# Performance work log

Measured on AMD Instinct MI355X. Metric: run time of the kernel, lower is better.

Reference implementation:

```python
import jax, jax.numpy as jnp
import numpy as np

S, N, D, H = 4096, 16384, 768, 768  # n_slots, n_inputs, feature_size(=dim), mlp hidden
ITERS = 3
SCALE = D ** -0.5
LN_EPS = 1e-5  # torch LayerNorm default


def _ln(x, g, b):
    m = jnp.mean(x, axis=-1, keepdims=True)
    v = jnp.var(x, axis=-1, keepdims=True)
    return (x - m) * jax.lax.rsqrt(v + LN_EPS) * g + b


def setup_inputs() -> dict:
    key = jax.random.key(0)
    ks = jax.random.split(key, 16)
    w = lambda k, shp: jax.random.normal(k, shp, dtype=jnp.float32) * 0.02
    return {
        "cand_feat": jax.random.normal(ks[0], (S, D), dtype=jnp.float32),
        "pano_feat": jax.random.normal(ks[1], (N, D), dtype=jnp.float32),
        "Wq": w(ks[2], (D, D)), "bq": jnp.zeros((D,), jnp.float32),
        "Wk": w(ks[3], (D, D)), "bk": jnp.zeros((D,), jnp.float32),
        "Wv": w(ks[4], (D, D)), "bv": jnp.zeros((D,), jnp.float32),
        "W_ih": w(ks[5], (3 * D, D)), "b_ih": jnp.zeros((3 * D,), jnp.float32),
        "W_hh": w(ks[6], (3 * D, D)), "b_hh": jnp.zeros((3 * D,), jnp.float32),
        "W1": w(ks[7], (H, D)), "b1": jnp.zeros((H,), jnp.float32),
        "W2": w(ks[8], (D, H)), "b2": jnp.zeros((D,), jnp.float32),
        "g_in": jnp.ones((D,), jnp.float32), "be_in": jnp.zeros((D,), jnp.float32),
        "g_sl": jnp.ones((D,), jnp.float32), "be_sl": jnp.zeros((D,), jnp.float32),
        "g_ff": jnp.ones((D,), jnp.float32), "be_ff": jnp.zeros((D,), jnp.float32),
    }


def reference(cand_feat, pano_feat, Wq, bq, Wk, bk, Wv, bv,
              W_ih, b_ih, W_hh, b_hh, W1, b1, W2, b2,
              g_in, be_in, g_sl, be_sl, g_ff, be_ff):
    # dropout layers act as identity at inference
    slots = cand_feat                       # [S, D]
    pano = _ln(pano_feat, g_in, be_in)      # [N, D]
    k = pano @ Wk.T + bk                    # [N, D]
    v = pano @ Wv.T + bv                    # [N, D]
    for _ in range(ITERS):
        slots_prev = slots
        q = _ln(slots, g_sl, be_sl) @ Wq.T + bq          # [S, D]
        dots = jnp.einsum('id,jd->ij', q, k) * SCALE     # [S, N]
        attn = jax.nn.softmax(dots, axis=1)
        updates = jnp.einsum('jd,ij->id', v, attn)       # [S, D]
        # torch.nn.GRUCell(updates, slots_prev)
        gx = updates @ W_ih.T + b_ih                     # [S, 3D]
        gh = slots_prev @ W_hh.T + b_hh                  # [S, 3D]
        xr, xz, xn = jnp.split(gx, 3, axis=-1)
        hr, hz, hn = jnp.split(gh, 3, axis=-1)
        r = jax.nn.sigmoid(xr + hr)
        z = jax.nn.sigmoid(xz + hz)
        n = jnp.tanh(xn + r * hn)
        h = (1.0 - z) * n + z * slots_prev               # [S, D]
        ff = _ln(h, g_ff, be_ff)
        slots = h + (jax.nn.relu(ff @ W1.T + b1) @ W2.T + b2)
    return slots
```

## Files before the change

kernel.cpp:

```cpp
#include <hip/hip_runtime.h>
#include <cstdint>
#include <cstddef>

typedef __bf16 bf16;
typedef __bf16 bf16x8 __attribute__((ext_vector_type(8)));
typedef __bf16 bf16x4 __attribute__((ext_vector_type(4)));
typedef float f32x4 __attribute__((ext_vector_type(4)));
typedef long long i64;

#define S_DIM 4096
#define N_DIM 16384
#define D_DIM 768
#define NCHUNK 8192
#define NZ 8
#define KSLICE (NCHUNK / NZ)

static constexpr float SCALE = 0.03608439182435161f;

__device__ inline void gl_lds16(const void* g, void* l) {
  __builtin_amdgcn_global_load_lds((const __attribute__((address_space(1))) void*)g,
                                   (__attribute__((address_space(3))) void*)l, 16, 0, 0);
}

__device__ inline unsigned char to_fp8(float x) {
  int p = __builtin_amdgcn_cvt_pk_fp8_f32(x, x, 0, false);
  return (unsigned char)(p & 0xff);
}

struct GemmArgs {
  const bf16* A; const bf16* B;
  const float* bias;
  float* outF; bf16* outB; unsigned char* outP8;
  const float* res;
  float* lsum;
  int M, N, K, lda, ldb;
  float scale;
};

template<int EPIL>
__device__ __forceinline__ void gemm_core(const GemmArgs& g, const int bm, const int bn,
                                          bf16* sA, bf16* sB) {
  const int tid  = threadIdx.x;
  const int wave = tid >> 6;
  const int lane = tid & 63;
  const int quad = lane >> 4;
  const int l15  = lane & 15;
  const int wm = (wave >> 1) * 64;
  const int wn = (wave & 1) * 64;

  f32x4 acc[4][4];
#pragma unroll
  for (int t = 0; t < 4; ++t)
#pragma unroll
    for (int u = 0; u < 4; ++u) acc[t][u] = (f32x4){0.f, 0.f, 0.f, 0.f};

  const int s0 = wave * 64 + lane;
  const int s1 = 256 + s0;
  const size_t lda = (size_t)g.lda, ldb = (size_t)g.ldb;
  const bf16* gA0 = g.A + (size_t)(bm + (s0 >> 2)) * lda + (s0 & 3) * 8;
  const bf16* gA1 = g.A + (size_t)(bm + (s1 >> 2)) * lda + (s1 & 3) * 8;
  const bf16* gB0 = g.B + (size_t)(bn + (s0 >> 2)) * ldb + (s0 & 3) * 8;
  const bf16* gB1 = g.B + (size_t)(bn + (s1 >> 2)) * ldb + (s1 & 3) * 8;
  bf16* lA0 = sA + s0 * 8;  bf16* lA1 = sA + s1 * 8;
  bf16* lB0 = sB + s0 * 8;  bf16* lB1 = sB + s1 * 8;

  for (int k0 = 0; k0 < g.K; k0 += 32) {
    __syncthreads();
    gl_lds16(gA0 + k0, lA0);
    gl_lds16(gA1 + k0, lA1);
    gl_lds16(gB0 + k0, lB0);
    gl_lds16(gB1 + k0, lB1);
    __syncthreads();
    bf16x8 af[4], bv[4];
#pragma unroll
    for (int t = 0; t < 4; ++t)
      af[t] = *(const bf16x8*)(sA + (wm + t * 16 + l15) * 32 + quad * 8);
#pragma unroll
    for (int u = 0; u < 4; ++u)
      bv[u] = *(const bf16x8*)(sB + (wn + u * 16 + l15) * 32 + quad * 8);
#pragma unroll
    for (int t = 0; t < 4; ++t)
#pragma unroll
      for (int u = 0; u < 4; ++u)
        acc[t][u] = __builtin_amdgcn_mfma_f32_16x16x32_bf16(af[t], bv[u], acc[t][u], 0, 0, 0);
  }

  const int ldc = g.N;
#pragma unroll
  for (int t = 0; t < 4; ++t) {
    const int rbase = bm + wm + t * 16 + quad * 4;
    if (EPIL == 10) {
      float rsum[4] = {0.f, 0.f, 0.f, 0.f};
#pragma unroll
      for (int u = 0; u < 4; ++u) {
        const int col = bn + wn + u * 16 + l15;
#pragma unroll
        for (int r = 0; r < 4; ++r) {
          float e = __expf(acc[t][u][r] * g.scale);
          g.outP8[(size_t)(rbase + r) * ldc + col] = to_fp8(e);
          rsum[r] += e;
        }
      }
#pragma unroll
      for (int m = 1; m < 16; m <<= 1)
#pragma unroll
        for (int r = 0; r < 4; ++r) rsum[r] += __shfl_xor(rsum[r], m, 64);
      if (l15 == 0)
#pragma unroll
        for (int r = 0; r < 4; ++r) atomicAdd(&g.lsum[rbase + r], rsum[r]);
    } else {
#pragma unroll
      for (int u = 0; u < 4; ++u) {
        const int col = bn + wn + u * 16 + l15;
        const float cbias = (EPIL == 0 || EPIL == 4 || EPIL == 5) ? g.bias[col] : 0.f;
#pragma unroll
        for (int r = 0; r < 4; ++r) {
          const size_t idx = (size_t)(rbase + r) * ldc + col;
          const float v = acc[t][u][r];
          if (EPIL == 0) g.outB[idx] = (bf16)(v + cbias);
          else if (EPIL == 4) { float x = v + cbias; g.outB[idx] = (bf16)(x > 0.f ? x : 0.f); }
          else if (EPIL == 5) g.outF[idx] = v + cbias + g.res[idx];
          else if (EPIL == 9) g.outP8[idx] = to_fp8(v + g.bias[rbase + r]);
        }
      }
    }
  }
}

#define GEMM_SHARED __shared__ __align__(16) bf16 sA[128 * 32]; __shared__ __align__(16) bf16 sB[128 * 32]

__global__ __launch_bounds__(256) void k_dots(GemmArgs g) {
  GEMM_SHARED; gemm_core<10>(g, blockIdx.y * 128, blockIdx.x * 128, sA, sB);
}
__global__ __launch_bounds__(256) void k_qgemm(GemmArgs g) {
  GEMM_SHARED; gemm_core<0>(g, blockIdx.y * 128, blockIdx.x * 128, sA, sB);
}
__global__ __launch_bounds__(256) void k_kgemm(GemmArgs g) {
  GEMM_SHARED; gemm_core<0>(g, blockIdx.y * 128, blockIdx.x * 128, sA, sB);
}
__global__ __launch_bounds__(256) void k_vtgemm(GemmArgs g) {
  GEMM_SHARED; gemm_core<9>(g, blockIdx.y * 128, blockIdx.x * 128, sA, sB);
}
__global__ __launch_bounds__(256) void k_relu(GemmArgs g) {
  GEMM_SHARED; gemm_core<4>(g, blockIdx.y * 128, blockIdx.x * 128, sA, sB);
}
__global__ __launch_bounds__(256) void k_resid(GemmArgs g) {
  GEMM_SHARED; gemm_core<5>(g, blockIdx.y * 128, blockIdx.x * 128, sA, sB);
}
__global__ __launch_bounds__(256) void k_dual(GemmArgs a, GemmArgs b, int split) {
  GEMM_SHARED;
  if ((int)blockIdx.x < split) gemm_core<0>(a, blockIdx.y * 128, blockIdx.x * 128, sA, sB);
  else                         gemm_core<0>(b, blockIdx.y * 128, (blockIdx.x - split) * 128, sA, sB);
}

struct F8Args {
  const unsigned char* A; const unsigned char* B;
  bf16* out;
  int lda, ldb;
};

template<int INIT>
__global__ __launch_bounds__(256) void k_updsplit(F8Args u) {
  __shared__ __align__(16) unsigned char sA[128 * 32];
  __shared__ __align__(16) unsigned char sB[128 * 32];
  const int z = blockIdx.z;
  const unsigned char* A = u.A + (size_t)z * KSLICE;
  const unsigned char* B = u.B + (size_t)z * KSLICE;
  bf16* out = u.out + (size_t)z * S_DIM * D_DIM;

  const int tid  = threadIdx.x;
  const int wave = tid >> 6;
  const int lane = tid & 63;
  const int quad = lane >> 4;
  const int l15  = lane & 15;
  const int bm = blockIdx.y * 128;
  const int bn = blockIdx.x * 128;
  const int wm = (wave >> 1) * 64;
  const int wn = (wave & 1) * 64;

  f32x4 acc[4][4];
#pragma unroll
  for (int t = 0; t < 4; ++t)
#pragma unroll
    for (int u2 = 0; u2 < 4; ++u2) acc[t][u2] = (f32x4){0.f, 0.f, 0.f, 0.f};

  const int s0 = wave * 64 + lane;
  const size_t lda = (size_t)u.lda, ldb = (size_t)u.ldb;
  const unsigned char* gA0 = A + (size_t)(bm + (s0 >> 1)) * lda + (s0 & 1) * 16;
  const unsigned char* gB0 = B + (size_t)(bn + (s0 >> 1)) * ldb + (s0 & 1) * 16;
  unsigned char* lA0 = sA + s0 * 16;
  unsigned char* lB0 = sB + s0 * 16;

  for (int k0 = 0; k0 < KSLICE; k0 += 32) {
    __syncthreads();
    gl_lds16(gA0 + k0, lA0);
    gl_lds16(gB0 + k0, lB0);
    __syncthreads();
    i64 af[4], bv[4];
#pragma unroll
    for (int t = 0; t < 4; ++t)
      af[t] = *(const i64*)(sA + (wm + t * 16 + l15) * 32 + quad * 8);
#pragma unroll
    for (int u2 = 0; u2 < 4; ++u2)
      bv[u2] = *(const i64*)(sB + (wn + u2 * 16 + l15) * 32 + quad * 8);
#pragma unroll
    for (int t = 0; t < 4; ++t)
#pragma unroll
      for (int u2 = 0; u2 < 4; ++u2)
        acc[t][u2] = __builtin_amdgcn_mfma_f32_16x16x32_fp8_fp8(af[t], bv[u2], acc[t][u2], 0, 0, 0);
  }

#pragma unroll
  for (int t = 0; t < 4; ++t) {
    const int rbase = bm + wm + t * 16 + quad * 4;
#pragma unroll
    for (int u2 = 0; u2 < 4; ++u2) {
      const int col = bn + wn + u2 * 16 + l15;
#pragma unroll
      for (int r = 0; r < 4; ++r) {
        const size_t idx = (size_t)(rbase + r) * D_DIM + col;
        if (INIT) out[idx] = (bf16)acc[t][u2][r];
        else      out[idx] = (bf16)((float)out[idx] + acc[t][u2][r]);
      }
    }
  }
}

__global__ void reduce8_div_k(const bf16* __restrict__ bufs, const float* __restrict__ lsum,
                              bf16* __restrict__ out) {
  const int idx = blockIdx.x * 256 + threadIdx.x;
  const int row = idx / 192;
  const float inv = 1.0f / lsum[row];
  float s0 = 0.f, s1 = 0.f, s2 = 0.f, s3 = 0.f;
#pragma unroll
  for (int z = 0; z < NZ; ++z) {
    bf16x4 v = ((const bf16x4*)(bufs + (size_t)z * S_DIM * D_DIM))[idx];
    s0 += (float)v[0]; s1 += (float)v[1]; s2 += (float)v[2]; s3 += (float)v[3];
  }
  bf16x4 y;
  y[0] = (bf16)(s0 * inv); y[1] = (bf16)(s1 * inv);
  y[2] = (bf16)(s2 * inv); y[3] = (bf16)(s3 * inv);
  ((bf16x4*)out)[idx] = y;
}

__global__ void ln_stats_k(const float* __restrict__ X, float2* __restrict__ st) {
  const int row  = blockIdx.x * 4 + (threadIdx.x >> 6);
  const int lane = threadIdx.x & 63;
  const float4* xr = (const float4*)(X + (size_t)row * 768);
  float s = 0.f, ss = 0.f;
#pragma unroll
  for (int i = 0; i < 3; ++i) {
    float4 v = xr[lane + 64 * i];
    s  += v.x + v.y + v.z + v.w;
    ss += v.x * v.x + v.y * v.y + v.z * v.z + v.w * v.w;
  }
#pragma unroll
  for (int m = 1; m < 64; m <<= 1) { s += __shfl_xor(s, m, 64); ss += __shfl_xor(ss, m, 64); }
  if (lane == 0) {
    float mean = s * (1.f / 768.f);
    float var  = ss * (1.f / 768.f) - mean * mean;
    st[row] = make_float2(mean, rsqrtf(var + 1e-5f));
  }
}

__global__ void ln_apply_k(const float* __restrict__ X, const float2* __restrict__ st,
                           const float* __restrict__ gam, const float* __restrict__ bet,
                           bf16* __restrict__ Y) {
  const int idx = blockIdx.x * 256 + threadIdx.x;
  const int row = idx / 192, c4 = idx % 192;
  const float2 s = st[row];
  float4 x  = ((const float4*)(X + (size_t)row * 768))[c4];
  float4 g4 = ((const float4*)gam)[c4];
  float4 b4 = ((const float4*)bet)[c4];
  bf16x4 y;
  y[0] = (bf16)((x.x - s.x) * s.y * g4.x + b4.x);
  y[1] = (bf16)((x.y - s.x) * s.y * g4.y + b4.y);
  y[2] = (bf16)((x.z - s.x) * s.y * g4.z + b4.z);
  y[3] = (bf16)((x.w - s.x) * s.y * g4.w + b4.w);
  ((bf16x4*)(Y + (size_t)row * 768))[c4] = y;
}

__global__ void cvt_k(const float* __restrict__ X, bf16* __restrict__ Y) {
  const int i = blockIdx.x * 256 + threadIdx.x;
  float4 v = ((const float4*)X)[i];
  bf16x4 y;
  y[0] = (bf16)v.x; y[1] = (bf16)v.y; y[2] = (bf16)v.z; y[3] = (bf16)v.w;
  ((bf16x4*)Y)[i] = y;
}

__device__ inline float gru1(float xr, float xz, float xn, float hr, float hz, float hn, float sp) {
  float r = 1.f / (1.f + __expf(-(xr + hr)));
  float z = 1.f / (1.f + __expf(-(xz + hz)));
  float n = tanhf(xn + r * hn);
  return (1.f - z) * n + z * sp;
}

__global__ void gru_gate_k(const bf16* __restrict__ gx, const bf16* __restrict__ gh,
                           const float* __restrict__ slots, float* __restrict__ h) {
  const int idx = blockIdx.x * 256 + threadIdx.x;
  const int row = idx / 192, c4 = idx % 192;
  const bf16x4* gxr = (const bf16x4*)(gx + (size_t)row * 2304);
  const bf16x4* ghr = (const bf16x4*)(gh + (size_t)row * 2304);
  bf16x4 xr = gxr[c4], xz = gxr[192 + c4], xn = gxr[384 + c4];
  bf16x4 hr = ghr[c4], hz = ghr[192 + c4], hn = ghr[384 + c4];
  float4 sp = ((const float4*)(slots + (size_t)row * 768))[c4];
  float4 o;
  o.x = gru1((float)xr[0], (float)xz[0], (float)xn[0], (float)hr[0], (float)hz[0], (float)hn[0], sp.x);
  o.y = gru1((float)xr[1], (float)xz[1], (float)xn[1], (float)hr[1], (float)hz[1], (float)hn[1], sp.y);
  o.z = gru1((float)xr[2], (float)xz[2], (float)xn[2], (float)hr[2], (float)hz[2], (float)hn[2], sp.z);
  o.w = gru1((float)xr[3], (float)xz[3], (float)xn[3], (float)hr[3], (float)hz[3], (float)hn[3], sp.w);
  ((float4*)(h + (size_t)row * 768))[c4] = o;
}

extern "C" void kernel_launch(void* const* d_in, const int* in_sizes, int n_in,
                              void* d_out, int out_size, void* d_ws, size_t ws_size,
                              hipStream_t stream) {
  (void)in_sizes; (void)n_in; (void)out_size; (void)ws_size;
  const float* cand  = (const float*)d_in[0];
  const float* pano  = (const float*)d_in[1];
  const float* Wq  = (const float*)d_in[2];  const float* bq  = (const float*)d_in[3];
  const float* Wk  = (const float*)d_in[4];  const float* bk  = (const float*)d_in[5];
  const float* Wv  = (const float*)d_in[6];  const float* bv  = (const float*)d_in[7];
  const float* Wih = (const float*)d_in[8];  const float* bih = (const float*)d_in[9];
  const float* Whh = (const float*)d_in[10]; const float* bhh = (const float*)d_in[11];
  const float* W1  = (const float*)d_in[12]; const float* b1  = (const float*)d_in[13];
  const float* W2  = (const float*)d_in[14]; const float* b2  = (const float*)d_in[15];
  const float* g_in = (const float*)d_in[16]; const float* be_in = (const float*)d_in[17];
  const float* g_sl = (const float*)d_in[18]; const float* be_sl = (const float*)d_in[19];
  const float* g_ff = (const float*)d_in[20]; const float* be_ff = (const float*)d_in[21];

  const size_t WU = (size_t)D_DIM * D_DIM;

  char* base = (char*)d_ws;
  size_t off = 0;
  auto alloc = [&](size_t bytes) -> void* {
    void* r = base + off;
    off = (off + bytes + 255) & ~(size_t)255;
    return r;
  };

  bf16* wq_bf  = (bf16*)alloc(WU * 2);
  bf16* wk_bf  = (bf16*)alloc(WU * 2);
  bf16* wv_bf  = (bf16*)alloc(WU * 2);
  bf16* wih_bf = (bf16*)alloc(3 * WU * 2);
  bf16* whh_bf = (bf16*)alloc(3 * WU * 2);
  bf16* w1_bf  = (bf16*)alloc(WU * 2);
  bf16* w2_bf  = (bf16*)alloc(WU * 2);
  bf16* k_bf   = (bf16*)alloc((size_t)N_DIM * D_DIM * 2);
  unsigned char* vt_f8 = (unsigned char*)alloc((size_t)N_DIM * D_DIM);
  float* slots = (float*)alloc((size_t)S_DIM * D_DIM * 4);
  bf16* slots_bf = (bf16*)alloc((size_t)S_DIM * D_DIM * 2);
  float2* statsP = (float2*)alloc((size_t)N_DIM * 8);
  float2* statsS = (float2*)alloc((size_t)S_DIM * 8);
  bf16* slotsln = (bf16*)alloc((size_t)S_DIM * D_DIM * 2);
  bf16* q_bf    = (bf16*)alloc((size_t)S_DIM * D_DIM * 2);
  bf16* upd_bf  = (bf16*)alloc((size_t)S_DIM * D_DIM * 2);
  bf16* hln_bf  = (bf16*)alloc((size_t)S_DIM * D_DIM * 2);
  bf16* m1_bf   = (bf16*)alloc((size_t)S_DIM * D_DIM * 2);
  float* lsum   = (float*)alloc((size_t)S_DIM * 4);
  float* hbuf   = (float*)alloc((size_t)S_DIM * D_DIM * 4);
  const size_t PCH = (size_t)S_DIM * NCHUNK;
  const size_t PBF = (size_t)NZ * S_DIM * D_DIM * 2;
  char* arena = (char*)alloc(PCH + PBF);
  bf16* panoln = (bf16*)arena;
  unsigned char* Pchunk = (unsigned char*)arena;
  bf16* pbufs = (bf16*)(arena + PCH);
  bf16* gx = (bf16*)arena;
  bf16* gh = (bf16*)(arena + PCH);

  cvt_k<<<dim3(WU / 1024), 256, 0, stream>>>(Wq, wq_bf);
  cvt_k<<<dim3(WU / 1024), 256, 0, stream>>>(Wk, wk_bf);
  cvt_k<<<dim3(WU / 1024), 256, 0, stream>>>(Wv, wv_bf);
  cvt_k<<<dim3(3 * WU / 1024), 256, 0, stream>>>(Wih, wih_bf);
  cvt_k<<<dim3(3 * WU / 1024), 256, 0, stream>>>(Whh, whh_bf);
  cvt_k<<<dim3(WU / 1024), 256, 0, stream>>>(W1, w1_bf);
  cvt_k<<<dim3(WU / 1024), 256, 0, stream>>>(W2, w2_bf);

  ln_stats_k<<<dim3(N_DIM / 4), 256, 0, stream>>>(pano, statsP);
  ln_apply_k<<<dim3(N_DIM * 192 / 256), 256, 0, stream>>>(pano, statsP, g_in, be_in, panoln);
  {
    GemmArgs ak{};
    ak.A = panoln; ak.B = wk_bf; ak.bias = bk; ak.outB = k_bf;
    ak.M = N_DIM; ak.N = D_DIM; ak.K = D_DIM; ak.lda = D_DIM; ak.ldb = D_DIM;
    k_kgemm<<<dim3(6, 128), 256, 0, stream>>>(ak);
    GemmArgs av{};
    av.A = wv_bf; av.B = panoln; av.bias = bv; av.outP8 = vt_f8;
    av.M = D_DIM; av.N = N_DIM; av.K = D_DIM; av.lda = D_DIM; av.ldb = D_DIM;
    k_vtgemm<<<dim3(128, 6), 256, 0, stream>>>(av);
  }

  hipMemcpyAsync(slots, cand, (size_t)S_DIM * D_DIM * 4, hipMemcpyDeviceToDevice, stream);
  cvt_k<<<dim3(S_DIM * D_DIM / 1024), 256, 0, stream>>>(cand, slots_bf);

  for (int iter = 0; iter < 3; ++iter) {
    ln_stats_k<<<dim3(S_DIM / 4), 256, 0, stream>>>(slots, statsS);
    ln_apply_k<<<dim3(S_DIM * 192 / 256), 256, 0, stream>>>(slots, statsS, g_sl, be_sl, slotsln);
    GemmArgs aq{};
    aq.A = slotsln; aq.B = wq_bf; aq.bias = bq; aq.outB = q_bf;
    aq.M = S_DIM; aq.N = D_DIM; aq.K = D_DIM; aq.lda = D_DIM; aq.ldb = D_DIM;
    k_qgemm<<<dim3(6, 32), 256, 0, stream>>>(aq);

    hipMemsetAsync(lsum, 0, (size_t)S_DIM * 4, stream);
    for (int c = 0; c < N_DIM / NCHUNK; ++c) {
      GemmArgs ad{};
      ad.A = q_bf; ad.B = k_bf + (size_t)c * NCHUNK * D_DIM;
      ad.outP8 = Pchunk; ad.lsum = lsum; ad.scale = SCALE;
      ad.M = S_DIM; ad.N = NCHUNK; ad.K = D_DIM; ad.lda = D_DIM; ad.ldb = D_DIM;
      k_dots<<<dim3(NCHUNK / 128, S_DIM / 128), 256, 0, stream>>>(ad);

      F8Args au{};
      au.A = Pchunk; au.B = vt_f8 + (size_t)c * NCHUNK;
      au.out = pbufs; au.lda = NCHUNK; au.ldb = N_DIM;
      if (c == 0) k_updsplit<1><<<dim3(6, 32, NZ), 256, 0, stream>>>(au);
      else        k_updsplit<0><<<dim3(6, 32, NZ), 256, 0, stream>>>(au);
    }
    reduce8_div_k<<<dim3(S_DIM * 192 / 256), 256, 0, stream>>>(pbufs, lsum, upd_bf);

    {
      GemmArgs agx{};
      agx.A = upd_bf; agx.B = wih_bf; agx.bias = bih; agx.outB = gx;
      agx.M = S_DIM; agx.N = 3 * D_DIM; agx.K = D_DIM; agx.lda = D_DIM; agx.ldb = D_DIM;
      GemmArgs agh{};
      agh.A = slots_bf; agh.B = whh_bf; agh.bias = bhh; agh.outB = gh;
      agh.M = S_DIM; agh.N = 3 * D_DIM; agh.K = D_DIM; agh.lda = D_DIM; agh.ldb = D_DIM;
      k_dual<<<dim3(36, 32), 256, 0, stream>>>(agx, agh, 18);
    }
    gru_gate_k<<<dim3(S_DIM * 192 / 256), 256, 0, stream>>>(gx, gh, slots, hbuf);

    ln_stats_k<<<dim3(S_DIM / 4), 256, 0, stream>>>(hbuf, statsS);
    ln_apply_k<<<dim3(S_DIM * 192 / 256), 256, 0, stream>>>(hbuf, statsS, g_ff, be_ff, hln_bf);
    GemmArgs am1{};
    am1.A = hln_bf; am1.B = w1_bf; am1.bias = b1; am1.outB = m1_bf;
    am1.M = S_DIM; am1.N = D_DIM; am1.K = D_DIM; am1.lda = D_DIM; am1.ldb = D_DIM;
    k_relu<<<dim3(6, 32), 256, 0, stream>>>(am1);
    GemmArgs am2{};
    am2.A = m1_bf; am2.B = w2_bf; am2.bias = b2; am2.res = hbuf;
    am2.outF = (iter == 2) ? (float*)d_out : slots;
    am2.M = S_DIM; am2.N = D_DIM; am2.K = D_DIM; am2.lda = D_DIM; am2.ldb = D_DIM;
    k_resid<<<dim3(6, 32), 256, 0, stream>>>(am2);

    if (iter < 2)
      cvt_k<<<dim3(S_DIM * D_DIM / 1024), 256, 0, stream>>>(slots, slots_bf);
  }
}
```

Baseline: 1.903 ms.

## Swizzle LDS layouts, widen fp8 update tile, and halve split-K slices

```diff
diff --git a/kernel.cpp b/kernel.cpp
--- a/kernel.cpp
+++ b/kernel.cpp
@@ -12,7 +12,7 @@
 #define N_DIM 16384
 #define D_DIM 768
 #define NCHUNK 8192
-#define NZ 8
+#define NZ 4
 #define KSLICE (NCHUNK / NZ)
 
 static constexpr float SCALE = 0.03608439182435161f;
@@ -56,13 +56,18 @@
 
   const int s0 = wave * 64 + lane;
   const int s1 = 256 + s0;
+  const int r0 = s0 >> 2, c0 = s0 & 3, x0 = (r0 & 3) ^ ((r0 >> 2) & 3);
+  const int r1 = s1 >> 2, c1 = s1 & 3, x1 = (r1 & 3) ^ ((r1 >> 2) & 3);
   const size_t lda = (size_t)g.lda, ldb = (size_t)g.ldb;
-  const bf16* gA0 = g.A + (size_t)(bm + (s0 >> 2)) * lda + (s0 & 3) * 8;
-  const bf16* gA1 = g.A + (size_t)(bm + (s1 >> 2)) * lda + (s1 & 3) * 8;
-  const bf16* gB0 = g.B + (size_t)(bn + (s0 >> 2)) * ldb + (s0 & 3) * 8;
-  const bf16* gB1 = g.B + (size_t)(bn + (s1 >> 2)) * ldb + (s1 & 3) * 8;
+  const bf16* gA0 = g.A + (size_t)(bm + r0) * lda + (c0 ^ x0) * 8;
+  const bf16* gA1 = g.A + (size_t)(bm + r1) * lda + (c1 ^ x1) * 8;
+  const bf16* gB0 = g.B + (size_t)(bn + r0) * ldb + (c0 ^ x0) * 8;
+  const bf16* gB1 = g.B + (size_t)(bn + r1) * ldb + (c1 ^ x1) * 8;
   bf16* lA0 = sA + s0 * 8;  bf16* lA1 = sA + s1 * 8;
   bf16* lB0 = sB + s0 * 8;  bf16* lB1 = sB + s1 * 8;
+
+  const int xr = (l15 & 3) ^ ((l15 >> 2) & 3);
+  const int qx = (quad ^ xr) * 8;
 
   for (int k0 = 0; k0 < g.K; k0 += 32) {
     __syncthreads();
@@ -74,10 +79,10 @@
     bf16x8 af[4], bv[4];
 #pragma unroll
     for (int t = 0; t < 4; ++t)
-      af[t] = *(const bf16x8*)(sA + (wm + t * 16 + l15) * 32 + quad * 8);
+      af[t] = *(const bf16x8*)(sA + (wm + t * 16 + l15) * 32 + qx);
 #pragma unroll
     for (int u = 0; u < 4; ++u)
-      bv[u] = *(const bf16x8*)(sB + (wn + u * 16 + l15) * 32 + quad * 8);
+      bv[u] = *(const bf16x8*)(sB + (wn + u * 16 + l15) * 32 + qx);
 #pragma unroll
     for (int t = 0; t < 4; ++t)
 #pragma unroll
@@ -160,53 +165,62 @@
 };
 
 template<int INIT>
-__global__ __launch_bounds__(256) void k_updsplit(F8Args u) {
+__global__ __launch_bounds__(256) void k_upd(F8Args u) {
   __shared__ __align__(16) unsigned char sA[128 * 32];
-  __shared__ __align__(16) unsigned char sB[128 * 32];
-  const int z = blockIdx.z;
-  const unsigned char* A = u.A + (size_t)z * KSLICE;
-  const unsigned char* B = u.B + (size_t)z * KSLICE;
-  bf16* out = u.out + (size_t)z * S_DIM * D_DIM;
-
+  __shared__ __align__(16) unsigned char sB[256 * 32];
   const int tid  = threadIdx.x;
   const int wave = tid >> 6;
   const int lane = tid & 63;
   const int quad = lane >> 4;
   const int l15  = lane & 15;
   const int bm = blockIdx.y * 128;
-  const int bn = blockIdx.x * 128;
+  const int bn = blockIdx.x * 256;
+  const int z  = blockIdx.z;
   const int wm = (wave >> 1) * 64;
-  const int wn = (wave & 1) * 64;
-
-  f32x4 acc[4][4];
+  const int wn = (wave & 1) * 128;
+
+  const unsigned char* A = u.A + (size_t)z * KSLICE;
+  const unsigned char* B = u.B + (size_t)z * KSLICE;
+  bf16* out = u.out + (size_t)z * S_DIM * D_DIM;
+
+  f32x4 acc[4][8];
 #pragma unroll
   for (int t = 0; t < 4; ++t)
 #pragma unroll
-    for (int u2 = 0; u2 < 4; ++u2) acc[t][u2] = (f32x4){0.f, 0.f, 0.f, 0.f};
-
-  const int s0 = wave * 64 + lane;
+    for (int u2 = 0; u2 < 8; ++u2) acc[t][u2] = (f32x4){0.f, 0.f, 0.f, 0.f};
+
   const size_t lda = (size_t)u.lda, ldb = (size_t)u.ldb;
-  const unsigned char* gA0 = A + (size_t)(bm + (s0 >> 1)) * lda + (s0 & 1) * 16;
-  const unsigned char* gB0 = B + (size_t)(bn + (s0 >> 1)) * ldb + (s0 & 1) * 16;
-  unsigned char* lA0 = sA + s0 * 16;
-  unsigned char* lB0 = sB + s0 * 16;
+  const int ra = tid >> 1, ha = tid & 1;
+  const unsigned char* gA = A + (size_t)(bm + ra) * lda + ((ha ^ ((ra >> 2) & 1)) * 16);
+  unsigned char* lA = sA + tid * 16;
+  const int rb0 = tid >> 1, hb0 = tid & 1;
+  const int sb1 = tid + 256;
+  const int rb1 = sb1 >> 1, hb1 = sb1 & 1;
+  const unsigned char* gB0 = B + (size_t)(bn + rb0) * ldb + ((hb0 ^ ((rb0 >> 2) & 1)) * 16);
+  const unsigned char* gB1 = B + (size_t)(bn + rb1) * ldb + ((hb1 ^ ((rb1 >> 2) & 1)) * 16);
+  unsigned char* lB0 = sB + tid * 16;
+  unsigned char* lB1 = sB + sb1 * 16;
+
+  const int xh = (l15 >> 2) & 1;
+  const int qoff = (((quad >> 1) ^ xh) * 16) + (quad & 1) * 8;
 
   for (int k0 = 0; k0 < KSLICE; k0 += 32) {
     __syncthreads();
-    gl_lds16(gA0 + k0, lA0);
+    gl_lds16(gA + k0, lA);
     gl_lds16(gB0 + k0, lB0);
+    gl_lds16(gB1 + k0, lB1);
     __syncthreads();
-    i64 af[4], bv[4];
+    i64 af[4], bv[8];
 #pragma unroll
     for (int t = 0; t < 4; ++t)
-      af[t] = *(const i64*)(sA + (wm + t * 16 + l15) * 32 + quad * 8);
-#pragma unroll
-    for (int u2 = 0; u2 < 4; ++u2)
-      bv[u2] = *(const i64*)(sB + (wn + u2 * 16 + l15) * 32 + quad * 8);
+      af[t] = *(const i64*)(sA + (wm + t * 16 + l15) * 32 + qoff);
+#pragma unroll
+    for (int u2 = 0; u2 < 8; ++u2)
+      bv[u2] = *(const i64*)(sB + (wn + u2 * 16 + l15) * 32 + qoff);
 #pragma unroll
     for (int t = 0; t < 4; ++t)
 #pragma unroll
-      for (int u2 = 0; u2 < 4; ++u2)
+      for (int u2 = 0; u2 < 8; ++u2)
         acc[t][u2] = __builtin_amdgcn_mfma_f32_16x16x32_fp8_fp8(af[t], bv[u2], acc[t][u2], 0, 0, 0);
   }
 
@@ -214,7 +228,7 @@
   for (int t = 0; t < 4; ++t) {
     const int rbase = bm + wm + t * 16 + quad * 4;
 #pragma unroll
-    for (int u2 = 0; u2 < 4; ++u2) {
+    for (int u2 = 0; u2 < 8; ++u2) {
       const int col = bn + wn + u2 * 16 + l15;
 #pragma unroll
       for (int r = 0; r < 4; ++r) {
@@ -226,8 +240,8 @@
   }
 }
 
-__global__ void reduce8_div_k(const bf16* __restrict__ bufs, const float* __restrict__ lsum,
-                              bf16* __restrict__ out) {
+__global__ void reduce_div_k(const bf16* __restrict__ bufs, const float* __restrict__ lsum,
+                             bf16* __restrict__ out) {
   const int idx = blockIdx.x * 256 + threadIdx.x;
   const int row = idx / 192;
   const float inv = 1.0f / lsum[row];
@@ -330,6 +344,7 @@
   const float* g_ff = (const float*)d_in[20]; const float* be_ff = (const float*)d_in[21];
 
   const size_t WU = (size_t)D_DIM * D_DIM;
+  const size_t MB = 1024 * 1024;
 
   char* base = (char*)d_ws;
   size_t off = 0;
@@ -358,7 +373,6 @@
   bf16* hln_bf  = (bf16*)alloc((size_t)S_DIM * D_DIM * 2);
   bf16* m1_bf   = (bf16*)alloc((size_t)S_DIM * D_DIM * 2);
   float* lsum   = (float*)alloc((size_t)S_DIM * 4);
-  float* hbuf   = (float*)alloc((size_t)S_DIM * D_DIM * 4);
   const size_t PCH = (size_t)S_DIM * NCHUNK;
   const size_t PBF = (size_t)NZ * S_DIM * D_DIM * 2;
   char* arena = (char*)alloc(PCH + PBF);
@@ -366,7 +380,9 @@
   unsigned char* Pchunk = (unsigned char*)arena;
   bf16* pbufs = (bf16*)(arena + PCH);
   bf16* gx = (bf16*)arena;
-  bf16* gh = (bf16*)(arena + PCH);
+  bf16* gh = (bf16*)(arena + (size_t)S_DIM * 3 * D_DIM * 2);
+  float* hbuf = (float*)(arena + 2 * (size_t)S_DIM * 3 * D_DIM * 2);
+  (void)MB;
 
   cvt_k<<<dim3(WU / 1024), 256, 0, stream>>>(Wq, wq_bf);
   cvt_k<<<dim3(WU / 1024), 256, 0, stream>>>(Wk, wk_bf);
@@ -411,10 +427,10 @@
       F8Args au{};
       au.A = Pchunk; au.B = vt_f8 + (size_t)c * NCHUNK;
       au.out = pbufs; au.lda = NCHUNK; au.ldb = N_DIM;
-      if (c == 0) k_updsplit<1><<<dim3(6, 32, NZ), 256, 0, stream>>>(au);
-      else        k_updsplit<0><<<dim3(6, 32, NZ), 256, 0, stream>>>(au);
+      if (c == 0) k_upd<1><<<dim3(3, 32, NZ), 256, 0, stream>>>(au);
+      else        k_upd<0><<<dim3(3, 32, NZ), 256, 0, stream>>>(au);
     }
-    reduce8_div_k<<<dim3(S_DIM * 192 / 256), 256, 0, stream>>>(pbufs, lsum, upd_bf);
+    reduce_div_k<<<dim3(S_DIM * 192 / 256), 256, 0, stream>>>(pbufs, lsum, upd_bf);
 
     {
       GemmArgs agx{};
```

Result: slower. 2.021 ms (+6.2%).
